# Optimization experiments

Hardware: AMD Instinct MI355X
Metric: run time of the kernel (lower is better)

Reference implementation:

```python
import jax, jax.numpy as jnp
import numpy as np

N_ATOMS = 200000   # total atoms across batch of molecules
N_BONDS = 400000   # total directed bonds
HSIZE   = 256      # mpn_size
MLP     = 512      # mlp_size
BS_OUT  = 5        # bond edit classes (bs_outdim)
N_MOLS  = 1000     # batch of molecules (len(atom_scope))


def _p(k, shape, scale):
    return jax.random.normal(k, shape, jnp.float32) * scale


def setup_inputs() -> dict:
    key = jax.random.key(0)
    ks = jax.random.split(key, 12)
    s_h = 1.0 / np.sqrt(HSIZE).astype(np.float32)
    s_2h = 1.0 / np.sqrt(2 * HSIZE).astype(np.float32)
    s_m = 1.0 / np.sqrt(MLP).astype(np.float32)
    return {
        'c_atom':  jax.random.normal(ks[0], (N_ATOMS, HSIZE), jnp.float32),
        'ha_prev': jax.random.normal(ks[1], (N_ATOMS, HSIZE), jnp.float32),
        'W_vv':    jnp.eye(HSIZE, dtype=jnp.float32),  # nn.init.eye_ in original
        'W_vc':    _p(ks[2], (HSIZE, HSIZE), s_h),
        'bond_W1': _p(ks[3], (2 * HSIZE, MLP), s_2h),
        'bond_b1': jnp.zeros((MLP,), jnp.float32),
        'bond_W2': _p(ks[4], (MLP, BS_OUT), s_m),
        'bond_b2': jnp.zeros((BS_OUT,), jnp.float32),
        'uni_W1':  _p(ks[5], (HSIZE, MLP), s_h),
        'uni_b1':  jnp.zeros((MLP,), jnp.float32),
        'uni_W2':  _p(ks[6], (MLP, 1), s_m),
        'uni_b2':  jnp.zeros((1,), jnp.float32),
        'done_W1': _p(ks[7], (HSIZE, MLP), s_h),
        'done_b1': jnp.zeros((MLP,), jnp.float32),
        'done_W2': _p(ks[8], (MLP, 1), s_m),
        'done_b2': jnp.zeros((1,), jnp.float32),
        'mol_id':     jax.random.randint(ks[9], (N_ATOMS,), 0, N_MOLS, jnp.int32),
        'bond_index': jax.random.randint(ks[10], (N_BONDS, 2), 0, N_ATOMS, jnp.int32),
    }


def _mlp(x, W1, b1, W2, b2):
    # build_mlp: Linear -> ReLU -> (dropout, off at eval) -> Linear
    return jax.nn.relu(x @ W1 + b1) @ W2 + b2


def reference(c_atom, ha_prev, W_vv, W_vc,
              bond_W1, bond_b1, bond_W2, bond_b2,
              uni_W1, uni_b1, uni_W2, uni_b2,
              done_W1, done_b1, done_W2, done_b2,
              mol_id, bond_index):
    # ha = relu(W_vv @ ha_prev + W_vc @ c_atom); ha[0] = 0 (padding atom)
    ha = jax.nn.relu(ha_prev @ W_vv + c_atom @ W_vc)
    ha = ha.at[0].set(0.0)
    # per-molecule pooling (replaces python loop over atom_scope)
    hm = jax.ops.segment_sum(ha, mol_id, num_segments=N_MOLS)  # [N_MOLS, H]
    # gather bond endpoint embeddings (index_select_ND)
    bond_in = jnp.concatenate([ha[bond_index[:, 0]], ha[bond_index[:, 1]]], axis=-1)  # [E, 2H]
    bond_logits = _mlp(bond_in, bond_W1, bond_b1, bond_W2, bond_b2)  # [E, BS_OUT]
    uni_logits = _mlp(ha, uni_W1, uni_b1, uni_W2, uni_b2)            # [N, 1]
    done_logits = _mlp(hm, done_W1, done_b1, done_W2, done_b2)       # [M, 1]
    # edit_logits in original is a ragged per-mol concat of these three;
    # return the dense flat concatenation (same values, fixed shape)
    return jnp.concatenate([bond_logits.ravel(), uni_logits.ravel(), done_logits.ravel()])
```

## Files before the change

kernel.cpp:

```cpp
#include <hip/hip_runtime.h>
#include <hip/hip_bf16.h>
#include <math.h>

typedef __attribute__((ext_vector_type(8))) short bf16x8;
typedef __attribute__((ext_vector_type(4))) float f32x4;

static __device__ __forceinline__ unsigned short f2bf(float f) {
    union { float f; unsigned u; } v; v.f = f;
    unsigned r = v.u + 0x7fffu + ((v.u >> 16) & 1u);
    return (unsigned short)(r >> 16);
}

#define GLOAD16(g, l) __builtin_amdgcn_global_load_lds( \
    (const __attribute__((address_space(1))) void*)(g), \
    (__attribute__((address_space(3))) void*)(l), 16, 0, 0)

#if defined(__has_builtin)
#  if __has_builtin(__builtin_amdgcn_cvt_pk_fp8_f32) && __has_builtin(__builtin_amdgcn_cvt_pk_f32_fp8)
#    define HAVE_FP8_CVT 1
#  endif
#endif
#ifndef HAVE_FP8_CVT
#  define HAVE_FP8_CVT 0
#endif

static __device__ __forceinline__ float f8dec_sw(unsigned b) {
    unsigned s = b >> 7, e = (b >> 3) & 15, m = b & 7;
    float v = e ? ldexpf((float)(8 + m), (int)e - 10) : ldexpf((float)m, -9);
    return s ? -v : v;
}
static __device__ __forceinline__ unsigned char f8enc_sw(float x) {
    union { float f; unsigned u; } v; v.f = x;
    unsigned s = (v.u >> 31) << 7;
    float ax = fabsf(x);
    if (ax >= 448.f) return (unsigned char)(s | 0x7E);
    if (ax < 0.015625f) { int m = (int)(ax * 512.f + 0.5f); return (unsigned char)(s | m); }
    int e; float fr = frexpf(ax, &e);
    int q = (int)(fr * 16.f + 0.5f);
    if (q == 16) { q = 8; e += 1; }
    if (e - 1 > 8) return (unsigned char)(s | 0x7E);
    return (unsigned char)(s | ((e - 1 + 7) << 3) | (q - 8));
}
static __device__ __forceinline__ unsigned char f8e(float v) {
#if HAVE_FP8_CVT
    return (unsigned char)(__builtin_amdgcn_cvt_pk_fp8_f32(v, v, 0, false) & 0xFF);
#else
    return f8enc_sw(v);
#endif
}
static __device__ __forceinline__ void f8d2_lo(unsigned w, float& x, float& y) {
#if HAVE_FP8_CVT
    auto r = __builtin_amdgcn_cvt_pk_f32_fp8((int)w, false);
    x = r[0]; y = r[1];
#else
    x = f8dec_sw(w & 0xFF); y = f8dec_sw((w >> 8) & 0xFF);
#endif
}
static __device__ __forceinline__ void f8d2_hi(unsigned w, float& x, float& y) {
#if HAVE_FP8_CVT
    auto r = __builtin_amdgcn_cvt_pk_f32_fp8((int)w, true);
    x = r[0]; y = r[1];
#else
    x = f8dec_sw((w >> 16) & 0xFF); y = f8dec_sw((w >> 24) & 0xFF);
#endif
}

__global__ __launch_bounds__(256) void conv_weights(
    const float* __restrict__ Wvv, const float* __restrict__ Wvc,
    const float* __restrict__ bW1, const float* __restrict__ uW1,
    unsigned short* __restrict__ WcT, unsigned short* __restrict__ WgT)
{
    int idx = blockIdx.x * 256 + threadIdx.x;
    if (idx < 131072) {
        int n = idx & 255, k = idx >> 8;
        float s = (k < 256) ? Wvv[k * 256 + n] : Wvc[(k - 256) * 256 + n];
        WcT[((k >> 3) * 256 + n) * 8 + (k & 7)] = f2bf(s);
    } else {
        int t = idx - 131072;
        int k = t / 1536, n2 = t - k * 1536;
        float s;
        if (n2 < 512)       s = bW1[k * 512 + n2];
        else if (n2 < 1024) s = bW1[(256 + k) * 512 + (n2 - 512)];
        else                s = uW1[k * 512 + (n2 - 1024)];
        WgT[((k >> 3) * 1536 + n2) * 8 + (k & 7)] = f2bf(s);
    }
}

__global__ __launch_bounds__(512, 4) void ha_kernel(
    const float* __restrict__ ha_prev, const float* __restrict__ c_atom,
    const unsigned short* __restrict__ WcT, const int* __restrict__ mol_id,
    unsigned short* __restrict__ haB, float* __restrict__ hm, int NA)
{
    __shared__ __align__(16) unsigned short As[2][128 * 64];

    const int tid = threadIdx.x;
    const int wv = tid >> 6, lane = tid & 63;
    const int wr = wv >> 2, wc = wv & 3;
    const int c15 = lane & 15, kq = lane >> 4;
    const int xm3 = (c15 & 7) << 3;
    const int m0 = blockIdx.x * 128;

    const int cr0 = tid >> 3, chc = tid & 7;
    const int cr1 = (512 + tid) >> 3;
    int row0 = m0 + cr0; if (row0 >= NA) row0 = NA - 1;
    int row1 = m0 + cr1; if (row1 >= NA) row1 = NA - 1;

    f32x4 v00, v01, v10, v11;
    #define HA_LOAD(ks) { \
        const float* src = ((ks) < 4) ? ha_prev : c_atom; \
        const int kb = ((ks) & 3) * 64 + chc * 8; \
        const float* s0 = src + (size_t)row0 * 256 + kb; \
        const float* s1 = src + (size_t)row1 * 256 + kb; \
        v00 = *(const f32x4*)s0; v01 = *(const f32x4*)(s0 + 4); \
        v10 = *(const f32x4*)s1; v11 = *(const f32x4*)(s1 + 4); }
    #define HA_WRITE(buf) { \
        bf16x8 p0, p1; \
        p0[0]=(short)f2bf(v00[0]); p0[1]=(short)f2bf(v00[1]); p0[2]=(short)f2bf(v00[2]); p0[3]=(short)f2bf(v00[3]); \
        p0[4]=(short)f2bf(v01[0]); p0[5]=(short)f2bf(v01[1]); p0[6]=(short)f2bf(v01[2]); p0[7]=(short)f2bf(v01[3]); \
        p1[0]=(short)f2bf(v10[0]); p1[1]=(short)f2bf(v10[1]); p1[2]=(short)f2bf(v10[2]); p1[3]=(short)f2bf(v10[3]); \
        p1[4]=(short)f2bf(v11[0]); p1[5]=(short)f2bf(v11[1]); p1[6]=(short)f2bf(v11[2]); p1[7]=(short)f2bf(v11[3]); \
        *(bf16x8*)&As[buf][cr0 * 64 + ((chc * 8) ^ ((cr0 & 7) << 3))] = p0; \
        *(bf16x8*)&As[buf][cr1 * 64 + ((chc * 8) ^ ((cr1 & 7) << 3))] = p1; }

    f32x4 acc[4][4];
#pragma unroll
    for (int m = 0; m < 4; ++m)
#pragma unroll
        for (int n = 0; n < 4; ++n) acc[m][n] = (f32x4){0.f, 0.f, 0.f, 0.f};

    HA_LOAD(0); HA_WRITE(0);
    __syncthreads();

    for (int ks = 0; ks < 8; ++ks) {
        if (ks < 7) HA_LOAD(ks + 1);
        const int buf = ks & 1;
#pragma unroll
        for (int kk = 0; kk < 2; ++kk) {
            bf16x8 aF[4], bF[4];
            const int plane = ks * 8 + kk * 4 + kq;
#pragma unroll
            for (int n = 0; n < 4; ++n)
                bF[n] = *(const bf16x8*)(WcT + ((size_t)plane * 256 + wc * 64 + n * 16 + c15) * 8);
#pragma unroll
            for (int m = 0; m < 4; ++m)
                aF[m] = *(const bf16x8*)&As[buf][(wr * 64 + m * 16 + c15) * 64 + ((kk * 32 + kq * 8) ^ xm3)];
#pragma unroll
            for (int m = 0; m < 4; ++m)
#pragma unroll
                for (int n = 0; n < 4; ++n)
                    acc[m][n] = __builtin_amdgcn_mfma_f32_16x16x32_bf16(aF[m], bF[n], acc[m][n], 0, 0, 0);
        }
        if (ks < 7) HA_WRITE((ks + 1) & 1);
        __syncthreads();
    }

#pragma unroll
    for (int m = 0; m < 4; ++m) {
#pragma unroll
        for (int reg = 0; reg < 4; ++reg) {
            int row = m0 + wr * 64 + m * 16 + kq * 4 + reg;
            if (row >= NA) continue;
            bool z = (row == 0);
            int mol = z ? 0 : mol_id[row];
#pragma unroll
            for (int n = 0; n < 4; ++n) {
                int col = wc * 64 + n * 16 + c15;
                float v = fmaxf(acc[m][n][reg], 0.f);
                if (z) v = 0.f;
                haB[(size_t)row * 256 + col] = f2bf(v);
                if (!z) atomicAdd(&hm[mol * 256 + col], v);
            }
        }
    }
}

__global__ __launch_bounds__(1024, 4) void g_kernel(
    const unsigned short* __restrict__ haB, const unsigned short* __restrict__ WgT,
    unsigned char* __restrict__ G, unsigned char* __restrict__ Hu, int NA)
{
    __shared__ __align__(16) unsigned short As[4][128][64];

    const int tid = threadIdx.x;
    const int wv = tid >> 6, lane = tid & 63;
    const int wr = wv >> 3, wc = wv & 7;
    const int c15 = lane & 15, kq = lane >> 4;
    const int a0 = blockIdx.x * 128;
    const int nb = blockIdx.y;

    {
        const int kt = wv >> 2;
        const int rsub = lane >> 3, csub = lane & 7;
#pragma unroll
        for (int j = 0; j < 4; ++j) {
            int rg = (wv & 3) * 4 + j;
            int r = rg * 8 + rsub;
            int ga = a0 + r; if (ga >= NA) ga = NA - 1;
            GLOAD16(haB + (size_t)ga * 256 + kt * 64 + (size_t)((csub ^ (r & 7)) * 8),
                    &As[kt][rg * 8][0]);
        }
    }
    __syncthreads();

    f32x4 acc[4][4];
#pragma unroll
    for (int m = 0; m < 4; ++m)
#pragma unroll
        for (int n = 0; n < 4; ++n) acc[m][n] = (f32x4){0.f, 0.f, 0.f, 0.f};

    bf16x8 breg[2][4];
#pragma unroll
    for (int n = 0; n < 4; ++n)
        breg[0][n] = *(const bf16x8*)(WgT + ((size_t)kq * 1536 + nb * 512 + wc * 64 + n * 16 + c15) * 8);

#pragma unroll
    for (int s = 0; s < 8; ++s) {
        if (s < 7) {
            const int pl = (s + 1) * 4 + kq;
#pragma unroll
            for (int n = 0; n < 4; ++n)
                breg[(s + 1) & 1][n] = *(const bf16x8*)(WgT + ((size_t)pl * 1536 + nb * 512 + wc * 64 + n * 16 + c15) * 8);
        }
        const int ks = s >> 1, kk = s & 1;
        bf16x8 aF[4];
#pragma unroll
        for (int m = 0; m < 4; ++m) {
            int r = wr * 64 + m * 16 + c15;
            aF[m] = *(const bf16x8*)&As[ks][r][((kk * 4 + kq) ^ (r & 7)) * 8];
        }
#pragma unroll
        for (int m = 0; m < 4; ++m)
#pragma unroll
            for (int n = 0; n < 4; ++n)
                acc[m][n] = __builtin_amdgcn_mfma_f32_16x16x32_bf16(aF[m], breg[s & 1][n], acc[m][n], 0, 0, 0);
    }

    unsigned char* dst; int rstride;
    if (nb < 2) { dst = G + nb * 512; rstride = 1024; }
    else        { dst = Hu;           rstride = 512;  }
#pragma unroll
    for (int m = 0; m < 4; ++m) {
#pragma unroll
        for (int reg = 0; reg < 4; ++reg) {
            int row = a0 + wr * 64 + m * 16 + kq * 4 + reg;
            if (row >= NA) continue;
#pragma unroll
            for (int n = 0; n < 4; ++n) {
                int col = wc * 64 + n * 16 + c15;
                dst[(size_t)row * rstride + col] = f8e(acc[m][n][reg]);
            }
        }
    }
}

__global__ __launch_bounds__(256) void bond_stream(
    const unsigned char* __restrict__ G, const int* __restrict__ bidx,
    const float* __restrict__ b1, const float* __restrict__ W2,
    const float* __restrict__ b2, float* __restrict__ outB, int NB, int nwaves)
{
    const int lane = threadIdx.x & 63;
    const int wid = (blockIdx.x * blockDim.x + threadIdx.x) >> 6;

    float b1c[8], w2c[8][5];
#pragma unroll
    for (int i = 0; i < 8; ++i) {
        int h = lane * 8 + i;
        b1c[i] = b1[h];
#pragma unroll
        for (int j = 0; j < 5; ++j) w2c[i][j] = W2[h * 5 + j];
    }
    float bb[5];
#pragma unroll
    for (int j = 0; j < 5; ++j) bb[j] = b2[j];

    int e = wid;
    if (e >= NB) return;
    int2 ep = ((const int2*)bidx)[e];
    int2 epN = (e + nwaves < NB) ? ((const int2*)bidx)[e + nwaves] : ep;
    uint2 ga = *(const uint2*)(G + (size_t)ep.x * 1024 + lane * 8);
    uint2 gb = *(const uint2*)(G + (size_t)ep.y * 1024 + 512 + lane * 8);

    while (e < NB) {
        int en = e + nwaves;
        uint2 gaN, gbN; int2 epN2 = epN;
        if (en < NB) {
            gaN = *(const uint2*)(G + (size_t)epN.x * 1024 + lane * 8);
            gbN = *(const uint2*)(G + (size_t)epN.y * 1024 + 512 + lane * 8);
            int e2 = en + nwaves;
            if (e2 < NB) epN2 = ((const int2*)bidx)[e2];
        }
        float s[5] = {0.f, 0.f, 0.f, 0.f, 0.f};
#pragma unroll
        for (int half = 0; half < 2; ++half) {
            unsigned wa = half ? ga.y : ga.x;
            unsigned wb = half ? gb.y : gb.x;
            float a0v, a1v, a2v, a3v, b0v, b1v, b2v, b3v;
            f8d2_lo(wa, a0v, a1v); f8d2_hi(wa, a2v, a3v);
            f8d2_lo(wb, b0v, b1v); f8d2_hi(wb, b2v, b3v);
            float hv[4] = { a0v + b0v, a1v + b1v, a2v + b2v, a3v + b3v };
#pragma unroll
            for (int t = 0; t < 4; ++t) {
                int i = half * 4 + t;
                float p = fmaxf(hv[t] + b1c[i], 0.f);
#pragma unroll
                for (int j = 0; j < 5; ++j) s[j] += p * w2c[i][j];
            }
        }
#pragma unroll
        for (int off = 1; off < 64; off <<= 1)
#pragma unroll
            for (int j = 0; j < 5; ++j) s[j] += __shfl_xor(s[j], off);
        if (lane == 0) {
#pragma unroll
            for (int j = 0; j < 5; ++j) outB[(size_t)e * 5 + j] = s[j] + bb[j];
        }
        e = en; ga = gaN; gb = gbN; epN = epN2;
    }
}

__global__ __launch_bounds__(256) void uni_stream(
    const unsigned char* __restrict__ Hu, const float* __restrict__ b1,
    const float* __restrict__ W2, const float* __restrict__ b2,
    float* __restrict__ outU, int NA, int nwaves)
{
    const int lane = threadIdx.x & 63;
    const int wid = (blockIdx.x * blockDim.x + threadIdx.x) >> 6;

    float b1c[8], w2c[8];
#pragma unroll
    for (int i = 0; i < 8; ++i) {
        int h = lane * 8 + i;
        b1c[i] = b1[h];
        w2c[i] = W2[h];
    }
    float bb = b2[0];

    for (int a = wid; a < NA; a += nwaves) {
        uint2 g = *(const uint2*)(Hu + (size_t)a * 512 + lane * 8);
        float s = 0.f;
#pragma unroll
        for (int half = 0; half < 2; ++half) {
            unsigned w = half ? g.y : g.x;
            float v0, v1, v2, v3;
            f8d2_lo(w, v0, v1); f8d2_hi(w, v2, v3);
            float hv[4] = { v0, v1, v2, v3 };
#pragma unroll
            for (int t = 0; t < 4; ++t) {
                int i = half * 4 + t;
                s += fmaxf(hv[t] + b1c[i], 0.f) * w2c[i];
            }
        }
#pragma unroll
        for (int off = 1; off < 64; off <<= 1) s += __shfl_xor(s, off);
        if (lane == 0) outU[a] = s + bb;
    }
}

__global__ __launch_bounds__(512, 4) void bond_gemm(
    const unsigned short* __restrict__ haB, const int* __restrict__ bidx,
    const unsigned short* __restrict__ WgT, const float* __restrict__ b1,
    const float* __restrict__ W2, const float* __restrict__ b2,
    float* __restrict__ outB, int NB)
{
    __shared__ __align__(16) unsigned short As[8 * 64 * 64];
    __shared__ float obuf[64][5];

    const int tid = threadIdx.x;
    const int wv = tid >> 6, lane = tid & 63;
    const int c15 = lane & 15, kq = lane >> 4;
    const int b0 = blockIdx.x * 64;

    if (tid < 320) ((float*)obuf)[tid] = 0.f;

    {
        const int ep = wv >> 2, koff = (wv & 3) * 64;
        const int rsub = lane >> 3, csub = lane & 7;
        int eidxs[8];
#pragma unroll
        for (int j = 0; j < 8; ++j) {
            int gbd = b0 + j * 8 + rsub; if (gbd >= NB) gbd = 0;
            eidxs[j] = bidx[gbd * 2 + ep];
        }
#pragma unroll
        for (int j = 0; j < 8; ++j) {
            int r = j * 8 + rsub;
            GLOAD16(haB + (size_t)eidxs[j] * 256 + koff + (size_t)((csub ^ (r & 7)) * 8),
                    As + wv * 4096 + j * 512);
        }
    }
    __syncthreads();

    f32x4 acc[4][4];
#pragma unroll
    for (int m = 0; m < 4; ++m)
#pragma unroll
        for (int n = 0; n < 4; ++n) acc[m][n] = (f32x4){0.f, 0.f, 0.f, 0.f};

    bf16x8 breg[2][4];
#pragma unroll
    for (int n = 0; n < 4; ++n)
        breg[0][n] = *(const bf16x8*)(WgT + ((size_t)(kq & 31) * 1536 + (kq >> 5) * 512 + wv * 64 + n * 16 + c15) * 8);
#pragma unroll
    for (int s = 0; s < 16; ++s) {
        if (s < 15) {
            const int pl = (s + 1) * 4 + kq;
#pragma unroll
            for (int n = 0; n < 4; ++n)
                breg[(s + 1) & 1][n] = *(const bf16x8*)(WgT + ((size_t)(pl & 31) * 1536 + (pl >> 5) * 512 + wv * 64 + n * 16 + c15) * 8);
        }
        const int ks = s >> 1, kk = s & 1;
        bf16x8 aF[4];
#pragma unroll
        for (int m = 0; m < 4; ++m) {
            int r = m * 16 + c15;
            aF[m] = *(const bf16x8*)&As[ks * 4096 + r * 64 + (((kk * 4 + kq) ^ (r & 7)) * 8)];
        }
#pragma unroll
        for (int m = 0; m < 4; ++m)
#pragma unroll
            for (int n = 0; n < 4; ++n)
                acc[m][n] = __builtin_amdgcn_mfma_f32_16x16x32_bf16(aF[m], breg[s & 1][n], acc[m][n], 0, 0, 0);
    }

    float b1c[4], w2c[4][5];
#pragma unroll
    for (int n = 0; n < 4; ++n) {
        int col = wv * 64 + n * 16 + c15;
        b1c[n] = b1[col];
#pragma unroll
        for (int j = 0; j < 5; ++j) w2c[n][j] = W2[col * 5 + j];
    }
#pragma unroll
    for (int m = 0; m < 4; ++m) {
#pragma unroll
        for (int reg = 0; reg < 4; ++reg) {
            float s[5] = {0.f, 0.f, 0.f, 0.f, 0.f};
#pragma unroll
            for (int n = 0; n < 4; ++n) {
                float p = fmaxf(acc[m][n][reg] + b1c[n], 0.f);
#pragma unroll
                for (int j = 0; j < 5; ++j) s[j] += p * w2c[n][j];
            }
#pragma unroll
            for (int off = 1; off < 16; off <<= 1)
#pragma unroll
                for (int j = 0; j < 5; ++j) s[j] += __shfl_xor(s[j], off);
            if (c15 == 0) {
                int rl = m * 16 + kq * 4 + reg;
#pragma unroll
                for (int j = 0; j < 5; ++j) atomicAdd(&obuf[rl][j], s[j]);
            }
        }
    }
    __syncthreads();
    {
        int r = tid >> 3, j = tid & 7;
        if (j < 5) {
            int row = b0 + r;
            if (row < NB) outB[(size_t)row * 5 + j] = obuf[r][j] + b2[j];
        }
    }
}

__global__ __launch_bounds__(512, 4) void uni_kernel(
    const unsigned short* __restrict__ haB, const unsigned short* __restrict__ WgT,
    const float* __restrict__ b1, const float* __restrict__ W2,
    const float* __restrict__ b2, float* __restrict__ outU, int NA)
{
    __shared__ __align__(16) unsigned short As[4 * 64 * 64];
    __shared__ float obuf[64];

    const int tid = threadIdx.x;
    const int wv = tid >> 6, lane = tid & 63;
    const int c15 = lane & 15, kq = lane >> 4;
    const int a0 = blockIdx.x * 64;

    if (tid < 64) obuf[tid] = 0.f;

    {
        const int kt = wv >> 1, koff = kt * 64;
        const int rsub = lane >> 3, csub = lane & 7;
#pragma unroll
        for (int jj = 0; jj < 4; ++jj) {
            int j = (wv & 1) * 4 + jj;
            int r = j * 8 + rsub;
            int ga = a0 + r; if (ga >= NA) ga = NA - 1;
            GLOAD16(haB + (size_t)ga * 256 + koff + (size_t)((csub ^ (r & 7)) * 8),
                    As + kt * 4096 + j * 512);
        }
    }
    __syncthreads();

    f32x4 acc[4][4];
#pragma unroll
    for (int m = 0; m < 4; ++m)
#pragma unroll
        for (int n = 0; n < 4; ++n) acc[m][n] = (f32x4){0.f, 0.f, 0.f, 0.f};

    bf16x8 breg[2][4];
#pragma unroll
    for (int n = 0; n < 4; ++n)
        breg[0][n] = *(const bf16x8*)(WgT + ((size_t)kq * 1536 + 1024 + wv * 64 + n * 16 + c15) * 8);
#pragma unroll
    for (int s = 0; s < 8; ++s) {
        if (s < 7) {
            const int pl = (s + 1) * 4 + kq;
#pragma unroll
            for (int n = 0; n < 4; ++n)
                breg[(s + 1) & 1][n] = *(const bf16x8*)(WgT + ((size_t)pl * 1536 + 1024 + wv * 64 + n * 16 + c15) * 8);
        }
        const int ks = s >> 1, kk = s & 1;
        bf16x8 aF[4];
#pragma unroll
        for (int m = 0; m < 4; ++m) {
            int r = m * 16 + c15;
            aF[m] = *(const bf16x8*)&As[ks * 4096 + r * 64 + (((kk * 4 + kq) ^ (r & 7)) * 8)];
        }
#pragma unroll
        for (int m = 0; m < 4; ++m)
#pragma unroll
            for (int n = 0; n < 4; ++n)
                acc[m][n] = __builtin_amdgcn_mfma_f32_16x16x32_bf16(aF[m], breg[s & 1][n], acc[m][n], 0, 0, 0);
    }

    float b1c[4], w2c[4];
#pragma unroll
    for (int n = 0; n < 4; ++n) {
        int col = wv * 64 + n * 16 + c15;
        b1c[n] = b1[col];
        w2c[n] = W2[col];
    }
#pragma unroll
    for (int m = 0; m < 4; ++m) {
#pragma unroll
        for (int reg = 0; reg < 4; ++reg) {
            float s = 0.f;
#pragma unroll
            for (int n = 0; n < 4; ++n)
                s += fmaxf(acc[m][n][reg] + b1c[n], 0.f) * w2c[n];
#pragma unroll
            for (int off = 1; off < 16; off <<= 1) s += __shfl_xor(s, off);
            if (c15 == 0) atomicAdd(&obuf[m * 16 + kq * 4 + reg], s);
        }
    }
    __syncthreads();
    if (tid < 64) {
        int row = a0 + tid;
        if (row < NA) outU[row] = obuf[tid] + b2[0];
    }
}

__global__ __launch_bounds__(256) void done_kernel(
    const float* __restrict__ hm, const float* __restrict__ W1,
    const float* __restrict__ b1, const float* __restrict__ W2,
    const float* __restrict__ b2, float* __restrict__ outD, int NM)
{
    __shared__ float rsh[4][256];
    __shared__ float red[4][4];
    const int tid = threadIdx.x;
    const int wv = tid >> 6, lane = tid & 63;
    const int mol0 = blockIdx.x * 4;
#pragma unroll
    for (int q = 0; q < 4; ++q)
        rsh[q][tid] = (mol0 + q < NM) ? hm[(size_t)(mol0 + q) * 256 + tid] : 0.f;
    __syncthreads();
    float h[4][2];
#pragma unroll
    for (int q = 0; q < 4; ++q) { h[q][0] = 0.f; h[q][1] = 0.f; }
    for (int k = 0; k < 256; ++k) {
        float w0 = W1[k * 512 + tid];
        float w1 = W1[k * 512 + tid + 256];
#pragma unroll
        for (int q = 0; q < 4; ++q) {
            h[q][0] += rsh[q][k] * w0;
            h[q][1] += rsh[q][k] * w1;
        }
    }
    float bb0 = b1[tid], bb1v = b1[tid + 256];
    float ww0 = W2[tid], ww1 = W2[tid + 256];
#pragma unroll
    for (int q = 0; q < 4; ++q) {
        float p = fmaxf(h[q][0] + bb0, 0.f) * ww0 + fmaxf(h[q][1] + bb1v, 0.f) * ww1;
#pragma unroll
        for (int off = 1; off < 64; off <<= 1) p += __shfl_xor(p, off);
        if (lane == 0) red[q][wv] = p;
    }
    __syncthreads();
    if (tid < 4 && mol0 + tid < NM)
        outD[mol0 + tid] = red[tid][0] + red[tid][1] + red[tid][2] + red[tid][3] + b2[0];
}

extern "C" void kernel_launch(void* const* d_in, const int* in_sizes, int n_in,
                              void* d_out, int out_size, void* d_ws, size_t ws_size,
                              hipStream_t stream)
{
    const float* c_atom  = (const float*)d_in[0];
    const float* ha_prev = (const float*)d_in[1];
    const float* W_vv    = (const float*)d_in[2];
    const float* W_vc    = (const float*)d_in[3];
    const float* bW1     = (const float*)d_in[4];
    const float* bb1     = (const float*)d_in[5];
    const float* bW2     = (const float*)d_in[6];
    const float* bb2     = (const float*)d_in[7];
    const float* uW1     = (const float*)d_in[8];
    const float* ub1     = (const float*)d_in[9];
    const float* uW2     = (const float*)d_in[10];
    const float* ub2     = (const float*)d_in[11];
    const float* dW1     = (const float*)d_in[12];
    const float* db1     = (const float*)d_in[13];
    const float* dW2     = (const float*)d_in[14];
    const float* db2     = (const float*)d_in[15];
    const int* mol_id    = (const int*)d_in[16];
    const int* bidx      = (const int*)d_in[17];

    const int H = 256, BS = 5;
    const int NA = in_sizes[0] / H;
    const int NB = in_sizes[17] / 2;
    const int NM = out_size - NB * BS - NA;

    float* out  = (float*)d_out;
    float* outB = out;
    float* outU = out + (size_t)NB * BS;
    float* outD = outU + NA;

    char* ws = (char*)d_ws;
    size_t off = 0;
    unsigned short* haB = (unsigned short*)(ws + off);
    off += (size_t)NA * H * 2;            off = (off + 255) & ~(size_t)255;
    float* hm = (float*)(ws + off);
    off += (size_t)NM * H * 4;            off = (off + 255) & ~(size_t)255;
    unsigned short* WcT = (unsigned short*)(ws + off);
    off += (size_t)131072 * 2;            off = (off + 255) & ~(size_t)255;
    unsigned short* WgT = (unsigned short*)(ws + off);
    off += (size_t)393216 * 2;            off = (off + 255) & ~(size_t)255;
    unsigned char* G = (unsigned char*)(ws + off);
    size_t need_G = off + (size_t)NA * 1024;
    size_t offHu = (need_G + 255) & ~(size_t)255;
    unsigned char* Hu = (unsigned char*)(ws + offHu);
    size_t need_Hu = offHu + (size_t)NA * 512;

    const bool hasG  = ws_size >= need_G;
    const bool hasHu = ws_size >= need_Hu;

    hipMemsetAsync(hm, 0, (size_t)NM * H * 4, stream);
    conv_weights<<<2048, 256, 0, stream>>>(W_vv, W_vc, bW1, uW1, WcT, WgT);
    ha_kernel<<<(NA + 127) / 128, 512, 0, stream>>>(ha_prev, c_atom, WcT, mol_id, haB, hm, NA);

    if (hasG) {
        g_kernel<<<dim3((NA + 127) / 128, hasHu ? 3 : 2), 1024, 0, stream>>>(haB, WgT, G, Hu, NA);
        bond_stream<<<2048, 256, 0, stream>>>(G, bidx, bb1, bW2, bb2, outB, NB, 2048 * 4);
        if (hasHu)
            uni_stream<<<1024, 256, 0, stream>>>(Hu, ub1, uW2, ub2, outU, NA, 1024 * 4);
        else
            uni_kernel<<<(NA + 63) / 64, 512, 0, stream>>>(haB, WgT, ub1, uW2, ub2, outU, NA);
    } else {
        bond_gemm<<<(NB + 63) / 64, 512, 0, stream>>>(haB, bidx, WgT, bb1, bW2, bb2, outB, NB);
        uni_kernel<<<(NA + 63) / 64, 512, 0, stream>>>(haB, WgT, ub1, uW2, ub2, outU, NA);
    }
    done_kernel<<<(NM + 3) / 4, 256, 0, stream>>>(hm, dW1, db1, dW2, db2, outD, NM);
}
```

Before: 697.5 us.

## Replace per-element atomic segment sum with counting-sort and per-molecule reduction

Removes the 51M float atomicAdds into hm from the ha GEMM epilogue. Instead it builds a histogram of mol_id, scans it and scatters atom indices into molecule-sorted order, then a per-molecule kernel sums bf16 ha rows. The cost is four extra small kernel launches, a single-block scan, and random row gathers of haB. hm now sums bf16-rounded values rather than fp32, which slightly changes precision.

```diff
diff --git a/kernel.cpp b/kernel.cpp
--- a/kernel.cpp
+++ b/kernel.cpp
@@ -88,8 +88,8 @@
 
 __global__ __launch_bounds__(512, 4) void ha_kernel(
     const float* __restrict__ ha_prev, const float* __restrict__ c_atom,
-    const unsigned short* __restrict__ WcT, const int* __restrict__ mol_id,
-    unsigned short* __restrict__ haB, float* __restrict__ hm, int NA)
+    const unsigned short* __restrict__ WcT,
+    unsigned short* __restrict__ haB, int NA)
 {
     __shared__ __align__(16) unsigned short As[2][128 * 64];
 
@@ -161,16 +161,91 @@
             int row = m0 + wr * 64 + m * 16 + kq * 4 + reg;
             if (row >= NA) continue;
             bool z = (row == 0);
-            int mol = z ? 0 : mol_id[row];
 #pragma unroll
             for (int n = 0; n < 4; ++n) {
                 int col = wc * 64 + n * 16 + c15;
                 float v = fmaxf(acc[m][n][reg], 0.f);
                 if (z) v = 0.f;
                 haB[(size_t)row * 256 + col] = f2bf(v);
-                if (!z) atomicAdd(&hm[mol * 256 + col], v);
             }
         }
+    }
+}
+
+__global__ __launch_bounds__(256) void hist_kernel(
+    const int* __restrict__ mol_id, int* __restrict__ bins, int NA)
+{
+    int i = blockIdx.x * 256 + threadIdx.x;
+    if (i < NA) atomicAdd(&bins[mol_id[i]], 1);
+}
+
+__global__ __launch_bounds__(1024) void scan_kernel(
+    const int* __restrict__ bins, int* __restrict__ offs,
+    int* __restrict__ cursor, int NM)
+{
+    __shared__ int buf[1024];
+    const int t = threadIdx.x;
+    int base = 0;
+    for (int c0 = 0; c0 < NM; c0 += 1024) {
+        int v = (c0 + t < NM) ? bins[c0 + t] : 0;
+        buf[t] = v;
+        __syncthreads();
+        for (int d = 1; d < 1024; d <<= 1) {
+            int x = (t >= d) ? buf[t - d] : 0;
+            __syncthreads();
+            buf[t] += x;
+            __syncthreads();
+        }
+        int incl = buf[t];
+        if (c0 + t < NM) {
+            int ex = base + incl - v;
+            offs[c0 + t] = ex;
+            cursor[c0 + t] = ex;
+        }
+        int tot = buf[1023];
+        __syncthreads();
+        base += tot;
+    }
+    if (t == 0) offs[NM] = base;
+}
+
+__global__ __launch_bounds__(256) void scatter_kernel(
+    const int* __restrict__ mol_id, int* __restrict__ cursor,
+    int* __restrict__ sorted, int NA)
+{
+    int i = blockIdx.x * 256 + threadIdx.x;
+    if (i < NA) {
+        int p = atomicAdd(&cursor[mol_id[i]], 1);
+        sorted[p] = i;
+    }
+}
+
+__global__ __launch_bounds__(256) void hm_kernel(
+    const unsigned short* __restrict__ haB, const int* __restrict__ sorted,
+    const int* __restrict__ offs, float* __restrict__ hm, int NM)
+{
+    __shared__ float red[256][2];
+    const int mol = blockIdx.x;
+    const int t = threadIdx.x;
+    const int sub = t >> 7, cp = t & 127;
+    const int s0 = offs[mol], s1 = offs[mol + 1];
+    float a0 = 0.f, a1 = 0.f;
+    for (int i = s0 + sub; i < s1; i += 2) {
+        int a = sorted[i];
+        unsigned w = *(const unsigned*)(haB + (size_t)a * 256 + cp * 2);
+        union { unsigned u; float f; } lo, hi;
+        lo.u = w << 16;
+        hi.u = w & 0xFFFF0000u;
+        a0 += lo.f;
+        a1 += hi.f;
+    }
+    red[t][0] = a0; red[t][1] = a1;
+    __syncthreads();
+    if (t < 128) {
+        float r0 = red[t][0] + red[t + 128][0];
+        float r1 = red[t][1] + red[t + 128][1];
+        float2* dst = (float2*)&hm[(size_t)mol * 256 + cp * 2];
+        *dst = make_float2(r0, r1);
     }
 }
 
@@ -632,6 +707,14 @@
     off += (size_t)131072 * 2;            off = (off + 255) & ~(size_t)255;
     unsigned short* WgT = (unsigned short*)(ws + off);
     off += (size_t)393216 * 2;            off = (off + 255) & ~(size_t)255;
+    int* bins = (int*)(ws + off);
+    off += (size_t)NM * 4;                off = (off + 255) & ~(size_t)255;
+    int* cursor = (int*)(ws + off);
+    off += (size_t)NM * 4;                off = (off + 255) & ~(size_t)255;
+    int* offs = (int*)(ws + off);
+    off += (size_t)(NM + 1) * 4;          off = (off + 255) & ~(size_t)255;
+    int* sorted = (int*)(ws + off);
+    off += (size_t)NA * 4;                off = (off + 255) & ~(size_t)255;
     unsigned char* G = (unsigned char*)(ws + off);
     size_t need_G = off + (size_t)NA * 1024;
     size_t offHu = (need_G + 255) & ~(size_t)255;
@@ -641,9 +724,13 @@
     const bool hasG  = ws_size >= need_G;
     const bool hasHu = ws_size >= need_Hu;
 
-    hipMemsetAsync(hm, 0, (size_t)NM * H * 4, stream);
+    hipMemsetAsync(bins, 0, (size_t)NM * 4, stream);
     conv_weights<<<2048, 256, 0, stream>>>(W_vv, W_vc, bW1, uW1, WcT, WgT);
-    ha_kernel<<<(NA + 127) / 128, 512, 0, stream>>>(ha_prev, c_atom, WcT, mol_id, haB, hm, NA);
+    hist_kernel<<<(NA + 255) / 256, 256, 0, stream>>>(mol_id, bins, NA);
+    scan_kernel<<<1, 1024, 0, stream>>>(bins, offs, cursor, NM);
+    scatter_kernel<<<(NA + 255) / 256, 256, 0, stream>>>(mol_id, cursor, sorted, NA);
+    ha_kernel<<<(NA + 127) / 128, 512, 0, stream>>>(ha_prev, c_atom, WcT, haB, NA);
+    hm_kernel<<<NM, 256, 0, stream>>>(haB, sorted, offs, hm, NM);
 
     if (hasG) {
         g_kernel<<<dim3((NA + 127) / 128, hasHu ? 3 : 2), 1024, 0, stream>>>(haB, WgT, G, Hu, NA);
```

Result: slower. 760.2 us (+9.0%).

## Fuse uni MLP and molecule pooling into g_kernel, drop Hu intermediate

Applied to the files above, without the earlier changes.

The per-atom uni MLP second layer now runs directly in g_kernel's third column block, reducing through shuffles and shared-memory atomics, so the fp8 Hu buffer and the separate uni_stream pass go away. The segment-sum pooling into hm moves from ha_kernel's epilogue into g_kernel. There it reads haB tiles already staged in LDS, is split across the three column blocks, and skips zero values. The fallback GEMM kernels also drop their register double-buffering of B fragments and stop unrolling the k-loop. This trades an extra kernel plus intermediate traffic for more epilogue work and global atomics inside g_kernel.

```diff
diff --git a/kernel.cpp b/kernel.cpp
--- a/kernel.cpp
+++ b/kernel.cpp
@@ -9,6 +9,10 @@
     union { float f; unsigned u; } v; v.f = f;
     unsigned r = v.u + 0x7fffu + ((v.u >> 16) & 1u);
     return (unsigned short)(r >> 16);
+}
+static __device__ __forceinline__ float bf2f(unsigned short b) {
+    union { unsigned u; float f; } v; v.u = ((unsigned)b) << 16;
+    return v.f;
 }
 
 #define GLOAD16(g, l) __builtin_amdgcn_global_load_lds( \
@@ -88,8 +92,8 @@
 
 __global__ __launch_bounds__(512, 4) void ha_kernel(
     const float* __restrict__ ha_prev, const float* __restrict__ c_atom,
-    const unsigned short* __restrict__ WcT, const int* __restrict__ mol_id,
-    unsigned short* __restrict__ haB, float* __restrict__ hm, int NA)
+    const unsigned short* __restrict__ WcT,
+    unsigned short* __restrict__ haB, int NA)
 {
     __shared__ __align__(16) unsigned short As[2][128 * 64];
 
@@ -161,14 +165,12 @@
             int row = m0 + wr * 64 + m * 16 + kq * 4 + reg;
             if (row >= NA) continue;
             bool z = (row == 0);
-            int mol = z ? 0 : mol_id[row];
 #pragma unroll
             for (int n = 0; n < 4; ++n) {
                 int col = wc * 64 + n * 16 + c15;
                 float v = fmaxf(acc[m][n][reg], 0.f);
                 if (z) v = 0.f;
                 haB[(size_t)row * 256 + col] = f2bf(v);
-                if (!z) atomicAdd(&hm[mol * 256 + col], v);
             }
         }
     }
@@ -176,9 +178,14 @@
 
 __global__ __launch_bounds__(1024, 4) void g_kernel(
     const unsigned short* __restrict__ haB, const unsigned short* __restrict__ WgT,
-    unsigned char* __restrict__ G, unsigned char* __restrict__ Hu, int NA)
+    const int* __restrict__ mol_id, float* __restrict__ hm,
+    unsigned char* __restrict__ G, float* __restrict__ outU,
+    const float* __restrict__ ub1, const float* __restrict__ uW2,
+    const float* __restrict__ ub2, int NA)
 {
     __shared__ __align__(16) unsigned short As[4][128][64];
+    __shared__ float obuf[128];
+    __shared__ int molS[128];
 
     const int tid = threadIdx.x;
     const int wv = tid >> 6, lane = tid & 63;
@@ -187,6 +194,10 @@
     const int a0 = blockIdx.x * 128;
     const int nb = blockIdx.y;
 
+    if (tid < 128) {
+        obuf[tid] = 0.f;
+        molS[tid] = (a0 + tid < NA) ? mol_id[a0 + tid] : 0;
+    }
     {
         const int kt = wv >> 2;
         const int rsub = lane >> 3, csub = lane & 7;
@@ -234,19 +245,63 @@
                 acc[m][n] = __builtin_amdgcn_mfma_f32_16x16x32_bf16(aF[m], breg[s & 1][n], acc[m][n], 0, 0, 0);
     }
 
-    unsigned char* dst; int rstride;
-    if (nb < 2) { dst = G + nb * 512; rstride = 1024; }
-    else        { dst = Hu;           rstride = 512;  }
-#pragma unroll
-    for (int m = 0; m < 4; ++m) {
-#pragma unroll
-        for (int reg = 0; reg < 4; ++reg) {
-            int row = a0 + wr * 64 + m * 16 + kq * 4 + reg;
-            if (row >= NA) continue;
-#pragma unroll
-            for (int n = 0; n < 4; ++n) {
-                int col = wc * 64 + n * 16 + c15;
-                dst[(size_t)row * rstride + col] = f8e(acc[m][n][reg]);
+    if (nb < 2) {
+#pragma unroll
+        for (int m = 0; m < 4; ++m) {
+#pragma unroll
+            for (int reg = 0; reg < 4; ++reg) {
+                int row = a0 + wr * 64 + m * 16 + kq * 4 + reg;
+                if (row >= NA) continue;
+#pragma unroll
+                for (int n = 0; n < 4; ++n) {
+                    int col = wc * 64 + n * 16 + c15;
+                    G[(size_t)row * 1024 + nb * 512 + col] = f8e(acc[m][n][reg]);
+                }
+            }
+        }
+    } else {
+        float b1c[4], w2c[4];
+#pragma unroll
+        for (int n = 0; n < 4; ++n) {
+            int col = wc * 64 + n * 16 + c15;
+            b1c[n] = ub1[col];
+            w2c[n] = uW2[col];
+        }
+#pragma unroll
+        for (int m = 0; m < 4; ++m) {
+#pragma unroll
+            for (int reg = 0; reg < 4; ++reg) {
+                float s0 = 0.f;
+#pragma unroll
+                for (int n = 0; n < 4; ++n)
+                    s0 += fmaxf(acc[m][n][reg] + b1c[n], 0.f) * w2c[n];
+#pragma unroll
+                for (int off = 1; off < 16; off <<= 1) s0 += __shfl_xor(s0, off);
+                if (c15 == 0)
+                    atomicAdd(&obuf[wr * 64 + m * 16 + kq * 4 + reg], s0);
+            }
+        }
+        __syncthreads();
+        if (tid < 128) {
+            int row = a0 + tid;
+            if (row < NA) outU[row] = obuf[tid] + ub2[0];
+        }
+    }
+
+    {
+        const int c0 = nb * 86;
+        const int c1 = (c0 + 86 < 256) ? c0 + 86 : 256;
+        const int rgp = tid >> 7, tc = tid & 127;
+        const int c = c0 + tc;
+        if (c < c1) {
+            const int kt2 = c >> 6, q = (c & 63) >> 3, jj = c & 7;
+#pragma unroll 4
+            for (int rr = rgp; rr < 128; rr += 8) {
+                int row = a0 + rr;
+                if (row > 0 && row < NA) {
+                    float v = bf2f(As[kt2][rr][((q ^ (rr & 7)) << 3) + jj]);
+                    if (v != 0.f) atomicAdd(&hm[molS[rr] * 256 + c], v);
+                }
             }
         }
     }
@@ -317,41 +372,19 @@
     }
 }
 
-__global__ __launch_bounds__(256) void uni_stream(
-    const unsigned char* __restrict__ Hu, const float* __restrict__ b1,
-    const float* __restrict__ W2, const float* __restrict__ b2,
-    float* __restrict__ outU, int NA, int nwaves)
-{
-    const int lane = threadIdx.x & 63;
-    const int wid = (blockIdx.x * blockDim.x + threadIdx.x) >> 6;
-
-    float b1c[8], w2c[8];
-#pragma unroll
-    for (int i = 0; i < 8; ++i) {
-        int h = lane * 8 + i;
-        b1c[i] = b1[h];
-        w2c[i] = W2[h];
-    }
-    float bb = b2[0];
-
-    for (int a = wid; a < NA; a += nwaves) {
-        uint2 g = *(const uint2*)(Hu + (size_t)a * 512 + lane * 8);
-        float s = 0.f;
-#pragma unroll
-        for (int half = 0; half < 2; ++half) {
-            unsigned w = half ? g.y : g.x;
-            float v0, v1, v2, v3;
-            f8d2_lo(w, v0, v1); f8d2_hi(w, v2, v3);
-            float hv[4] = { v0, v1, v2, v3 };
-#pragma unroll
-            for (int t = 0; t < 4; ++t) {
-                int i = half * 4 + t;
-                s += fmaxf(hv[t] + b1c[i], 0.f) * w2c[i];
-            }
-        }
-#pragma unroll
-        for (int off = 1; off < 64; off <<= 1) s += __shfl_xor(s, off);
-        if (lane == 0) outU[a] = s + bb;
+__global__ __launch_bounds__(256) void hm_fallback(
+    const unsigned short* __restrict__ haB, const int* __restrict__ mol_id,
+    float* __restrict__ hm, int NA)
+{
+    int idx = blockIdx.x * 256 + threadIdx.x;
+    int row = idx >> 6, c4 = (idx & 63) * 4;
+    if (row == 0 || row >= NA) return;
+    int mol = mol_id[row];
+    const unsigned short* p = haB + (size_t)row * 256 + c4;
+#pragma unroll
+    for (int j = 0; j < 4; ++j) {
+        float v = bf2f(p[j]);
+        if (v != 0.f) atomicAdd(&hm[mol * 256 + c4 + j], v);
     }
 }
 
@@ -395,20 +428,14 @@
 #pragma unroll
         for (int n = 0; n < 4; ++n) acc[m][n] = (f32x4){0.f, 0.f, 0.f, 0.f};
 
-    bf16x8 breg[2][4];
-#pragma unroll
-    for (int n = 0; n < 4; ++n)
-        breg[0][n] = *(const bf16x8*)(WgT + ((size_t)(kq & 31) * 1536 + (kq >> 5) * 512 + wv * 64 + n * 16 + c15) * 8);
-#pragma unroll
+#pragma unroll 1
     for (int s = 0; s < 16; ++s) {
-        if (s < 15) {
-            const int pl = (s + 1) * 4 + kq;
-#pragma unroll
-            for (int n = 0; n < 4; ++n)
-                breg[(s + 1) & 1][n] = *(const bf16x8*)(WgT + ((size_t)(pl & 31) * 1536 + (pl >> 5) * 512 + wv * 64 + n * 16 + c15) * 8);
-        }
+        const int pl = s * 4 + kq;
+        bf16x8 br[4], aF[4];
+#pragma unroll
+        for (int n = 0; n < 4; ++n)
+            br[n] = *(const bf16x8*)(WgT + ((size_t)(pl & 31) * 1536 + (pl >> 5) * 512 + wv * 64 + n * 16 + c15) * 8);
         const int ks = s >> 1, kk = s & 1;
-        bf16x8 aF[4];
 #pragma unroll
         for (int m = 0; m < 4; ++m) {
             int r = m * 16 + c15;
@@ -418,7 +445,7 @@
         for (int m = 0; m < 4; ++m)
 #pragma unroll
             for (int n = 0; n < 4; ++n)
-                acc[m][n] = __builtin_amdgcn_mfma_f32_16x16x32_bf16(aF[m], breg[s & 1][n], acc[m][n], 0, 0, 0);
+                acc[m][n] = __builtin_amdgcn_mfma_f32_16x16x32_bf16(aF[m], br[n], acc[m][n], 0, 0, 0);
     }
 
     float b1c[4], w2c[4][5];
@@ -496,20 +523,14 @@
 #pragma unroll
         for (int n = 0; n < 4; ++n) acc[m][n] = (f32x4){0.f, 0.f, 0.f, 0.f};
 
-    bf16x8 breg[2][4];
-#pragma unroll
-    for (int n = 0; n < 4; ++n)
-        breg[0][n] = *(const bf16x8*)(WgT + ((size_t)kq * 1536 + 1024 + wv * 64 + n * 16 + c15) * 8);
-#pragma unroll
+#pragma unroll 1
     for (int s = 0; s < 8; ++s) {
-        if (s < 7) {
-            const int pl = (s + 1) * 4 + kq;
-#pragma unroll
-            for (int n = 0; n < 4; ++n)
-                breg[(s + 1) & 1][n] = *(const bf16x8*)(WgT + ((size_t)pl * 1536 + 1024 + wv * 64 + n * 16 + c15) * 8);
-        }
+        const int pl = s * 4 + kq;
+        bf16x8 br[4], aF[4];
+#pragma unroll
+        for (int n = 0; n < 4; ++n)
+            br[n] = *(const bf16x8*)(WgT + ((size_t)pl * 1536 + 1024 + wv * 64 + n * 16 + c15) * 8);
         const int ks = s >> 1, kk = s & 1;
-        bf16x8 aF[4];
 #pragma unroll
         for (int m = 0; m < 4; ++m) {
             int r = m * 16 + c15;
@@ -519,7 +540,7 @@
         for (int m = 0; m < 4; ++m)
 #pragma unroll
             for (int n = 0; n < 4; ++n)
-                acc[m][n] = __builtin_amdgcn_mfma_f32_16x16x32_bf16(aF[m], breg[s & 1][n], acc[m][n], 0, 0, 0);
+                acc[m][n] = __builtin_amdgcn_mfma_f32_16x16x32_bf16(aF[m], br[n], acc[m][n], 0, 0, 0);
     }
 
     float b1c[4], w2c[4];
@@ -634,25 +655,19 @@
     off += (size_t)393216 * 2;            off = (off + 255) & ~(size_t)255;
     unsigned char* G = (unsigned char*)(ws + off);
     size_t need_G = off + (size_t)NA * 1024;
-    size_t offHu = (need_G + 255) & ~(size_t)255;
-    unsigned char* Hu = (unsigned char*)(ws + offHu);
-    size_t need_Hu = offHu + (size_t)NA * 512;
-
-    const bool hasG  = ws_size >= need_G;
-    const bool hasHu = ws_size >= need_Hu;
+
+    const bool hasG = ws_size >= need_G;
 
     hipMemsetAsync(hm, 0, (size_t)NM * H * 4, stream);
     conv_weights<<<2048, 256, 0, stream>>>(W_vv, W_vc, bW1, uW1, WcT, WgT);
-    ha_kernel<<<(NA + 127) / 128, 512, 0, stream>>>(ha_prev, c_atom, WcT, mol_id, haB, hm, NA);
+    ha_kernel<<<(NA + 127) / 128, 512, 0, stream>>>(ha_prev, c_atom, WcT, haB, NA);
 
     if (hasG) {
-        g_kernel<<<dim3((NA + 127) / 128, hasHu ? 3 : 2), 1024, 0, stream>>>(haB, WgT, G, Hu, NA);
+        g_kernel<<<dim3((NA + 127) / 128, 3), 1024, 0, stream>>>(
+            haB, WgT, mol_id, hm, G, outU, ub1, uW2, ub2, NA);
         bond_stream<<<2048, 256, 0, stream>>>(G, bidx, bb1, bW2, bb2, outB, NB, 2048 * 4);
-        if (hasHu)
-            uni_stream<<<1024, 256, 0, stream>>>(Hu, ub1, uW2, ub2, outU, NA, 1024 * 4);
-        else
-            uni_kernel<<<(NA + 63) / 64, 512, 0, stream>>>(haB, WgT, ub1, uW2, ub2, outU, NA);
     } else {
+        hm_fallback<<<(NA * 64 + 255) / 256, 256, 0, stream>>>(haB, mol_id, hm, NA);
         bond_gemm<<<(NB + 63) / 64, 512, 0, stream>>>(haB, bidx, WgT, bb1, bW2, bb2, outB, NB);
         uni_kernel<<<(NA + 63) / 64, 512, 0, stream>>>(haB, WgT, ub1, uW2, ub2, outU, NA);
     }
```

Result: faster. 651.2 us (-6.6%).
